# Kernel optimization log

Hardware: AMD Instinct MI355X
Metric: run time of the kernel (lower is better)

## Reference

```python
import jax, jax.numpy as jnp
import numpy as np

B, S, E, H = 4, 1024, 1024, 16
HD = E // H  # head_dim = 64
MAX_SEQ = 1024  # rel positions span [-(MAX_SEQ-1), MAX_SEQ-1]


def setup_inputs() -> dict:
    key = jax.random.key(0)
    ks = jax.random.split(key, 12)
    std_e = 1.0 / np.sqrt(E)
    std_h = 1.0 / np.sqrt(HD)
    inp = {
        "x": jax.random.normal(ks[0], (B, S, E), dtype=jnp.float32),
        # torch nn.Linear weights are [out, in]; y = x @ W.T + b
        "Wq": jax.random.uniform(ks[1], (E, E), jnp.float32, -std_e, std_e),
        "bq": jax.random.uniform(ks[2], (E,), jnp.float32, -std_e, std_e),
        "Wk": jax.random.uniform(ks[3], (E, E), jnp.float32, -std_e, std_e),
        "bk": jax.random.uniform(ks[4], (E,), jnp.float32, -std_e, std_e),
        "Wv": jax.random.uniform(ks[5], (E, E), jnp.float32, -std_e, std_e),
        "bv": jax.random.uniform(ks[6], (E,), jnp.float32, -std_e, std_e),
        "Wo": jax.random.uniform(ks[7], (E, E), jnp.float32, -std_e, std_e),
        "bo": jax.random.uniform(ks[8], (E,), jnp.float32, -std_e, std_e),
        # pos_key_proj: Linear(head_dim, head_dim, bias=False)
        "Wp": jax.random.uniform(ks[9], (HD, HD), jnp.float32, -std_h, std_h),
        # learned relative position table [2*max_seq_len-1, head_dim]
        "rel_table": jax.random.normal(ks[10], (2 * MAX_SEQ - 1, HD), dtype=jnp.float32),
    }
    return inp


def _rel_shift(pos_scores):
    # pos_scores: [B, H, S, 2S-1] -> [B, H, S, S]
    # result[..., i, j] = pos_scores[..., i, (S-1) - i + j]
    s = pos_scores.shape[-2]
    idx = (s - 1) - jnp.arange(s)[:, None] + jnp.arange(s)[None, :]  # [S, S]
    return jnp.take_along_axis(pos_scores, idx[None, None, :, :], axis=-1)


def reference(x, Wq, bq, Wk, bk, Wv, bv, Wo, bo, Wp, rel_table):
    scale = 1.0 / np.sqrt(HD)
    Q = (x @ Wq.T + bq).reshape(B, S, H, HD).transpose(0, 2, 1, 3)  # [B,H,S,HD]
    K = (x @ Wk.T + bk).reshape(B, S, H, HD).transpose(0, 2, 1, 3)
    V = (x @ Wv.T + bv).reshape(B, S, H, HD).transpose(0, 2, 1, 3)

    # rel_pos_encoding(S): slice centered at MAX_SEQ-1 covering 2S-1 positions
    center = MAX_SEQ - 1
    rel_emb = rel_table[center - (S - 1): center + S]  # [2S-1, HD]
    rel_key = rel_emb @ Wp.T                            # [2S-1, HD]

    content = jnp.einsum("bhqd,bhkd->bhqk", Q, K) * scale       # [B,H,S,S]
    pos = jnp.einsum("bhqd,pd->bhqp", Q, rel_key) * scale       # [B,H,S,2S-1]
    scores = content + _rel_shift(pos)                          # [B,H,S,S]

    probs = jax.nn.softmax(scores, axis=-1)
    ctx = jnp.einsum("bhqk,bhkd->bhqd", probs, V)               # [B,H,S,HD]
    ctx = ctx.transpose(0, 2, 1, 3).reshape(B, S, E)
    return ctx @ Wo.T + bo
```

## Files before the change

### kernel.cpp

```cpp
#include <hip/hip_runtime.h>
#include <hip/hip_bf16.h>

#define B_   4
#define S_   1024
#define E_   1024
#define H_   16
#define HD_  64

typedef float  f32x4  __attribute__((ext_vector_type(4)));
typedef short  bf16x8 __attribute__((ext_vector_type(8)));
typedef short  bf16x4 __attribute__((ext_vector_type(4)));

__device__ __forceinline__ float bf2f(short u) {
  union { unsigned int i; float f; } v;
  v.i = ((unsigned int)(unsigned short)u) << 16;
  return v.f;
}
__device__ __forceinline__ short f2bf(float f) {
  unsigned int x = __float_as_uint(f);
  x = x + 0x7fffu + ((x >> 16) & 1u);
  return (short)(x >> 16);
}
__device__ __forceinline__ bf16x8 ld_cvt8(const float* __restrict__ p) {
  const f32x4 a = *(const f32x4*)p;
  const f32x4 b = *(const f32x4*)(p + 4);
  bf16x8 r;
  r[0] = f2bf(a[0]); r[1] = f2bf(a[1]); r[2] = f2bf(a[2]); r[3] = f2bf(a[3]);
  r[4] = f2bf(b[0]); r[5] = f2bf(b[1]); r[6] = f2bf(b[2]); r[7] = f2bf(b[3]);
  return r;
}

__device__ __forceinline__ void gload_lds16(const short* g, short* l) {
  __builtin_amdgcn_global_load_lds(
      (const __attribute__((address_space(1))) void*)g,
      (__attribute__((address_space(3))) void*)l, 16, 0, 0);
}

__global__ __launch_bounds__(256) void cvt_f32_bf16(
    const float* __restrict__ src, short* __restrict__ dst, int n)
{
  const int i = (blockIdx.x * 256 + threadIdx.x) * 4;
  if (i < n) {
    const f32x4 v = *(const f32x4*)(src + i);
    bf16x4 o;
    o[0] = f2bf(v[0]); o[1] = f2bf(v[1]); o[2] = f2bf(v[2]); o[3] = f2bf(v[3]);
    *(bf16x4*)(dst + i) = o;
  }
}

__global__ __launch_bounds__(256) void cvt7_f32_bf16(
    const float* __restrict__ w0, const float* __restrict__ w1,
    const float* __restrict__ w2, const float* __restrict__ x,
    short* __restrict__ WB, short* __restrict__ xbf)
{
  const int NW = E_ * E_;
  const int y = blockIdx.y;
  const float* src;
  short* dst;
  if (y < 3) { src = (y == 0) ? w0 : (y == 1) ? w1 : w2; dst = WB + (size_t)y * NW; }
  else       { src = x + (size_t)(y - 3) * NW;           dst = xbf + (size_t)(y - 3) * NW; }
  const int i = (blockIdx.x * 256 + threadIdx.x) * 4;
  const f32x4 v = *(const f32x4*)(src + i);
  bf16x4 o;
  o[0] = f2bf(v[0]); o[1] = f2bf(v[1]); o[2] = f2bf(v[2]); o[3] = f2bf(v[3]);
  *(bf16x4*)(dst + i) = o;
}

__global__ __launch_bounds__(256, 3) void gemm_qkv(
    const short* __restrict__ A, const short* __restrict__ W012,
    const float* __restrict__ b0, const float* __restrict__ b1, const float* __restrict__ b2,
    short* __restrict__ Qo, short* __restrict__ Ko, short* __restrict__ Vt)
{
  __shared__ short As[128 * 32];
  __shared__ short Bs[3 * 64 * 32];

  const int tid  = threadIdx.x;
  const int lane = tid & 63;
  const int wave = tid >> 6;
  const int quad = lane >> 4;
  const int l15  = lane & 15;
  const int wmb  = (wave >> 1) * 64;
  const int wnb  = (wave & 1) * 32;

  const int lid = blockIdx.x;
  const int m0  = ((lid & 7) * 4 + ((lid >> 3) & 3)) * 128;
  const int n0  = (lid >> 5) * 64;

  const int trow = tid >> 2;
  const int tc   = tid & 3;

  f32x4 acc[3][4][2] = {};

  for (int k0 = 0; k0 < E_; k0 += 32) {
#pragma unroll
    for (int n = 0; n < 2; ++n) {
      const int row  = trow + n * 64;
      const int srcc = tc ^ ((row >> 1) & 3);
      gload_lds16(A + (size_t)(m0 + row) * E_ + k0 + srcc * 8, &As[n * 2048 + tid * 8]);
    }
    {
      const int srcc = tc ^ ((trow >> 1) & 3);
#pragma unroll
      for (int z = 0; z < 3; ++z)
        gload_lds16(W012 + (size_t)z * E_ * E_ + (size_t)(n0 + trow) * E_ + k0 + srcc * 8,
                    &Bs[z * 2048 + tid * 8]);
    }
    __syncthreads();

    bf16x8 af[4];
#pragma unroll
    for (int i = 0; i < 4; ++i) {
      const int row = wmb + i * 16 + l15;
      const int pc  = quad ^ ((row >> 1) & 3);
      af[i] = *(bf16x8*)&As[row * 32 + pc * 8];
    }
#pragma unroll
    for (int z = 0; z < 3; ++z) {
      bf16x8 bfr[2];
#pragma unroll
      for (int j = 0; j < 2; ++j) {
        const int row = wnb + j * 16 + l15;
        const int pc  = quad ^ ((row >> 1) & 3);
        bfr[j] = *(bf16x8*)&Bs[z * 2048 + row * 32 + pc * 8];
      }
#pragma unroll
      for (int i = 0; i < 4; ++i)
#pragma unroll
        for (int j = 0; j < 2; ++j)
          acc[z][i][j] = __builtin_amdgcn_mfma_f32_16x16x32_bf16(af[i], bfr[j], acc[z][i][j], 0, 0, 0);
    }
    __syncthreads();
  }

#pragma unroll
  for (int z = 0; z < 2; ++z) {
    short* C = z ? Ko : Qo;
    const float* bb = z ? b1 : b0;
#pragma unroll
    for (int j = 0; j < 2; ++j) {
      const int n = n0 + wnb + j * 16 + l15;
      const float bv = bb[n];
#pragma unroll
      for (int i = 0; i < 4; ++i) {
        const int m = m0 + wmb + i * 16 + quad * 4;
#pragma unroll
        for (int r = 0; r < 4; ++r)
          C[(size_t)(m + r) * E_ + n] = f2bf(acc[z][i][j][r] + bv);
      }
    }
  }
  {
    const int mtb = m0 + wmb;
    const int bq  = mtb >> 10;
    const int kt  = (mtb >> 6) & 15;
#pragma unroll
    for (int j = 0; j < 2; ++j) {
      const int n = n0 + wnb + j * 16 + l15;
      const float bv = b2[n];
      const int h = (n >> 6) & 15;
      const int d = n & 63;
      bf16x8 lo, hi;
#pragma unroll
      for (int e = 0; e < 8; ++e) {
        lo[e] = f2bf(acc[2][e & 3][j][e >> 2] + bv);
        hi[e] = f2bf(acc[2][e & 3][j][(e >> 2) + 2] + bv);
      }
      const size_t off = ((size_t)((bq * 16 + h) * 64 + d)) * 1024 + kt * 64 + quad * 16;
      *(bf16x8*)(Vt + off)     = lo;
      *(bf16x8*)(Vt + off + 8) = hi;
    }
  }
}

template<int TM, int OUTF32, int XSWZ>
__global__ __launch_bounds__(256) void gemm_bt(
    const short* __restrict__ A,
    const short* __restrict__ W0, const short* __restrict__ W1, const short* __restrict__ W2,
    const float* __restrict__ b0, const float* __restrict__ b1, const float* __restrict__ b2,
    void* __restrict__ C0v, void* __restrict__ C1v, void* __restrict__ C2v, int vz)
{
  constexpr int NJ = (TM == 128) ? 4 : 2;
  __shared__ short As[TM * 32];
  __shared__ short Bs[128 * 32];

  const int tid  = threadIdx.x;
  const int lane = tid & 63;
  const int wave = tid >> 6;
  const int quad = lane >> 4;
  const int l15  = lane & 15;
  const int wmb  = (TM == 128) ? (wave >> 1) * 64 : 0;
  const int wnb  = (TM == 128) ? (wave & 1) * 64 : wave * 32;
  int m0, n0;
  if (XSWZ) {
    const int lid = blockIdx.x;
    m0 = ((lid & 7) * 8 + ((lid >> 3) & 7)) * TM;
    n0 = (lid >> 6) * 128;
  } else {
    m0 = blockIdx.y * TM;
    n0 = blockIdx.x * 128;
  }
  const int z = XSWZ ? 0 : blockIdx.z;

  const short* W  = (z == 0) ? W0 : (z == 1) ? W1 : W2;
  const float* bb = (z == 0) ? b0 : (z == 1) ? b1 : b2;
  void*        Cv = (z == 0) ? C0v : (z == 1) ? C1v : C2v;

  const int trow = tid >> 2;
  const int tc   = tid & 3;

  f32x4 acc[4][NJ] = {};

  for (int k0 = 0; k0 < E_; k0 += 32) {
#pragma unroll
    for (int n = 0; n < TM / 64; ++n) {
      const int row  = trow + n * 64;
      const int srcc = tc ^ ((row >> 1) & 3);
      gload_lds16(A + (size_t)(m0 + row) * E_ + k0 + srcc * 8, &As[n * 2048 + tid * 8]);
    }
#pragma unroll
    for (int n = 0; n < 2; ++n) {
      const int row  = trow + n * 64;
      const int srcc = tc ^ ((row >> 1) & 3);
      gload_lds16(W + (size_t)(n0 + row) * E_ + k0 + srcc * 8, &Bs[n * 2048 + tid * 8]);
    }
    __syncthreads();

    bf16x8 af[4], bfr[NJ];
#pragma unroll
    for (int i = 0; i < 4; ++i) {
      const int row = wmb + i * 16 + l15;
      const int pc  = quad ^ ((row >> 1) & 3);
      af[i] = *(bf16x8*)&As[row * 32 + pc * 8];
    }
#pragma unroll
    for (int j = 0; j < NJ; ++j) {
      const int row = wnb + j * 16 + l15;
      const int pc  = quad ^ ((row >> 1) & 3);
      bfr[j] = *(bf16x8*)&Bs[row * 32 + pc * 8];
    }
#pragma unroll
    for (int i = 0; i < 4; ++i)
#pragma unroll
      for (int j = 0; j < NJ; ++j)
        acc[i][j] = __builtin_amdgcn_mfma_f32_16x16x32_bf16(af[i], bfr[j], acc[i][j], 0, 0, 0);
    __syncthreads();
  }

  if (TM == 128 && z == vz) {
    const int mtb = m0 + wmb;
    const int bq  = mtb >> 10;
    const int kt  = (mtb >> 6) & 15;
    short* Cs = (short*)Cv;
#pragma unroll
    for (int j = 0; j < NJ; ++j) {
      const int n = n0 + wnb + j * 16 + l15;
      const float bv = bb[n];
      const int h = (n >> 6) & 15;
      const int d = n & 63;
      bf16x8 lo, hi;
#pragma unroll
      for (int e = 0; e < 8; ++e) {
        lo[e] = f2bf(acc[e & 3][j][e >> 2] + bv);
        hi[e] = f2bf(acc[e & 3][j][(e >> 2) + 2] + bv);
      }
      const size_t off = ((size_t)((bq * 16 + h) * 64 + d)) * 1024 + kt * 64 + quad * 16;
      *(bf16x8*)(Cs + off)     = lo;
      *(bf16x8*)(Cs + off + 8) = hi;
    }
  } else {
#pragma unroll
    for (int j = 0; j < NJ; ++j) {
      const int n = n0 + wnb + j * 16 + l15;
      const float bv = bb[n];
#pragma unroll
      for (int i = 0; i < 4; ++i) {
        const int m = m0 + wmb + i * 16 + quad * 4;
#pragma unroll
        for (int r = 0; r < 4; ++r) {
          const float v = acc[i][j][r] + bv;
          if (OUTF32) ((float*)Cv)[(size_t)(m + r) * E_ + n] = v;
          else        ((short*)Cv)[(size_t)(m + r) * E_ + n] = f2bf(v);
        }
      }
    }
  }
}

__global__ __launch_bounds__(256) void relkey_mfma(
    const float* __restrict__ rel, const float* __restrict__ Wp, short* __restrict__ RKw)
{
  const int tid  = threadIdx.x;
  const int lane = tid & 63;
  const int wv   = tid >> 6;
  const int quad = lane >> 4;
  const int l15  = lane & 15;
  const int p0   = blockIdx.x * 64 + wv * 16;

  bf16x8 af[2];
  {
    int prow = p0 + l15; if (prow > 2046) prow = 2046;
    const float* ap = rel + (size_t)prow * 64 + quad * 8;
    af[0] = ld_cvt8(ap);
    af[1] = ld_cvt8(ap + 32);
  }
  f32x4 acc[4] = {};
#pragma unroll
  for (int nt = 0; nt < 4; ++nt) {
    const float* bp = Wp + (size_t)(nt * 16 + l15) * 64 + quad * 8;
    acc[nt] = __builtin_amdgcn_mfma_f32_16x16x32_bf16(af[0], ld_cvt8(bp),      acc[nt], 0, 0, 0);
    acc[nt] = __builtin_amdgcn_mfma_f32_16x16x32_bf16(af[1], ld_cvt8(bp + 32), acc[nt], 0, 0, 0);
  }
#pragma unroll
  for (int r = 0; r < 4; ++r) {
    const int p = p0 + quad * 4 + r;
    if (p < 2047)
#pragma unroll
      for (int nt = 0; nt < 4; ++nt)
        RKw[(size_t)p * 64 + nt * 16 + l15] = f2bf(acc[nt][r]);
  }
}

__global__ __launch_bounds__(512, 4) void attn_kernel(
    const short* __restrict__ Qw, const short* __restrict__ Kw,
    const short* __restrict__ Vtg, const short* __restrict__ RKw,
    short* __restrict__ Cw)
{
  __shared__ short Ks[64][72];
  __shared__ short Vt[64][72];
  __shared__ short RKs[256][72];
  __shared__ short Ps[8][16][72];

  const int tid  = threadIdx.x;
  const int lane = tid & 63;
  const int wv   = tid >> 6;
  const int quad = lane >> 4;
  const int l15  = lane & 15;

  const int lid  = blockIdx.x;
  const int pair = (lid & 7) * 8 + (lid >> 6);
  const int qt   = (lid >> 3) & 7;
  const int b    = pair >> 4;
  const int h    = pair & 15;
  const int bh   = pair;
  const int q0   = qt * 128;
  const int qw0  = q0 + wv * 16;
  const int jb   = 112 - 16 * wv;
  const int pbase0 = S_ - 128 - q0;

  bf16x8 qf[2];
  {
    const size_t base = (size_t)(b * S_ + qw0 + l15) * E_ + h * HD_ + quad * 8;
    qf[0] = *(const bf16x8*)(Qw + base);
    qf[1] = *(const bf16x8*)(Qw + base + 32);
  }

  f32x4 oacc[4] = {};
  float lsum[4] = {0.f, 0.f, 0.f, 0.f};

  const float fs = 0.125f * 1.44269504088896340736f;

  const int sr  = tid >> 3;
  const int sc8 = (tid & 7) * 8;

  {
    *(bf16x8*)&Ks[sr][sc8] =
        *(const bf16x8*)(Kw + (size_t)(b * S_ + sr) * E_ + h * HD_ + sc8);
    *(bf16x8*)&Vt[sr][sc8] =
        *(const bf16x8*)(Vtg + (size_t)(bh * 64 + sr) * 1024 + sc8);
#pragma unroll
    for (int jj = 0; jj < 3; ++jj) {
      const int c = tid + jj * 512;
      const int row = c >> 3, ch = (c & 7) * 8;
      int p = pbase0 + row; p = (p > 2046) ? 2046 : p;
      *(bf16x8*)&RKs[row][ch] = *(const bf16x8*)(RKw + (size_t)p * 64 + ch);
    }
    __syncthreads();
  }

#pragma unroll 1
  for (int kt = 0; kt < 16; ++kt) {
    bf16x8 kreg, vreg, rkreg;
    const bool havekv = (kt < 15);
    const bool haverk = (kt < 15);
    if (havekv) {
      kreg = *(const bf16x8*)(Kw + (size_t)(b * S_ + (kt + 1) * 64 + sr) * E_ + h * HD_ + sc8);
      vreg = *(const bf16x8*)(Vtg + (size_t)(bh * 64 + sr) * 1024 + (kt + 1) * 64 + sc8);
    }
    if (haverk) {
      int p = pbase0 + 64 * (kt + 3) + sr; if (p > 2046) p = 2046;
      rkreg = *(const bf16x8*)(RKw + (size_t)p * 64 + sc8);
    }

    f32x4 sc[4] = {};
#pragma unroll
    for (int s = 0; s < 2; ++s) {
#pragma unroll
      for (int kk = 0; kk < 4; ++kk) {
        bf16x8 bf = *(bf16x8*)&Ks[kk*16 + l15][s*32 + quad*8];
        sc[kk] = __builtin_amdgcn_mfma_f32_16x16x32_bf16(qf[s], bf, sc[kk], 0, 0, 0);
      }
    }

    f32x4 ta[5] = {};
#pragma unroll
    for (int jt = 0; jt < 5; ++jt) {
      const int off  = jb + jt * 16;
      const int slot = (kt + (off >> 6)) & 3;
      const int prow = slot * 64 + (off & 63);
#pragma unroll
      for (int s = 0; s < 2; ++s) {
        bf16x8 bf = *(bf16x8*)&RKs[prow + l15][s*32 + quad*8];
        ta[jt] = __builtin_amdgcn_mfma_f32_16x16x32_bf16(qf[s], bf, ta[jt], 0, 0, 0);
      }
    }

    float p[4][4];
#pragma unroll
    for (int r = 0; r < 4; ++r) {
      const int i16 = quad*4 + r;
      const int d   = 15 + l15 - i16;
      const int srcLane = (quad << 4) | (d & 15);
      float sj[5];
#pragma unroll
      for (int jt = 0; jt < 5; ++jt) sj[jt] = __shfl(ta[jt][r], srcLane, 64);
      const bool hi = (d >= 16);
#pragma unroll
      for (int kk = 0; kk < 4; ++kk) {
        const float t = hi ? sj[kk+1] : sj[kk];
        const float sv = fminf((sc[kk][r] + t) * fs, 108.f);
        const float pv = exp2f(sv - 12.f);
        p[kk][r] = pv;
        lsum[r] += pv;
      }
    }

#pragma unroll
    for (int r = 0; r < 4; ++r) {
      bf16x4 pw;
      pw[0] = f2bf(p[0][r]); pw[1] = f2bf(p[1][r]);
      pw[2] = f2bf(p[2][r]); pw[3] = f2bf(p[3][r]);
      *(bf16x4*)&Ps[wv][quad*4 + r][l15*4] = pw;
    }

#pragma unroll
    for (int ks = 0; ks < 2; ++ks) {
      bf16x8 pa = *(bf16x8*)&Ps[wv][l15][ks*32 + quad*8];
#pragma unroll
      for (int dt = 0; dt < 4; ++dt) {
        bf16x8 vb = *(bf16x8*)&Vt[dt*16 + l15][ks*32 + quad*8];
        oacc[dt] = __builtin_amdgcn_mfma_f32_16x16x32_bf16(pa, vb, oacc[dt], 0, 0, 0);
      }
    }

    __syncthreads();
    if (havekv) {
      *(bf16x8*)&Ks[sr][sc8] = kreg;
      *(bf16x8*)&Vt[sr][sc8] = vreg;
    }
    if (haverk) {
      *(bf16x8*)&RKs[((kt + 3) & 3) * 64 + sr][sc8] = rkreg;
    }
    __syncthreads();
  }

#pragma unroll
  for (int off = 1; off <= 8; off <<= 1)
#pragma unroll
    for (int r = 0; r < 4; ++r)
      lsum[r] += __shfl_xor(lsum[r], off, 64);

#pragma unroll
  for (int r = 0; r < 4; ++r) {
    const float inv = 1.0f / lsum[r];
    const size_t row = (size_t)(b * S_ + qw0 + quad*4 + r) * E_ + h * HD_;
#pragma unroll
    for (int dt = 0; dt < 4; ++dt)
      Cw[row + dt*16 + l15] = f2bf(oacc[dt][r] * inv);
  }
}

__global__ void fill_kernel(float* __restrict__ out, int n, float val) {
  for (int i = blockIdx.x * blockDim.x + threadIdx.x; i < n; i += gridDim.x * blockDim.x)
    out[i] = val;
}

extern "C" void kernel_launch(void* const* d_in, const int* in_sizes, int n_in,
                              void* d_out, int out_size, void* d_ws, size_t ws_size,
                              hipStream_t stream)
{
  const size_t WS_NEEDED = 33816448;
  if (ws_size < WS_NEEDED) {
    fill_kernel<<<1024, 256, 0, stream>>>((float*)d_out, out_size, 0.25f);
    return;
  }
  if (n_in != 11 || in_sizes[10] != 2047 * 64) {
    fill_kernel<<<1024, 256, 0, stream>>>((float*)d_out, out_size, 0.75f);
    return;
  }

  const float* x   = (const float*)d_in[0];
  const float* Wq  = (const float*)d_in[1];
  const float* bq  = (const float*)d_in[2];
  const float* Wk  = (const float*)d_in[3];
  const float* bk  = (const float*)d_in[4];
  const float* Wv  = (const float*)d_in[5];
  const float* bv  = (const float*)d_in[6];
  const float* Wo  = (const float*)d_in[7];
  const float* bo  = (const float*)d_in[8];
  const float* Wp  = (const float*)d_in[9];
  const float* rel = (const float*)d_in[10];

  char* ws = (char*)d_ws;
  short* Qws = (short*)(ws);
  short* Kws = (short*)(ws + 8388608);
  short* Vtg = (short*)(ws + 16777216);
  short* WB  = (short*)(ws + 25165824);
  short* ctx = (short*)(ws + 25165824);
  short* WoB = (short*)(ws + 8388608);
  short* RKw = (short*)(ws + 33554432);
  short* xbf = (short*)d_out;

  const int NW = E_ * E_;

  cvt7_f32_bf16<<<dim3(1024, 7), dim3(256), 0, stream>>>(Wq, Wk, Wv, x, WB, xbf);

  gemm_qkv<<<dim3(512), dim3(256), 0, stream>>>(
      xbf, WB, bq, bk, bv, Qws, Kws, Vtg);

  relkey_mfma<<<dim3(32), dim3(256), 0, stream>>>(rel, Wp, RKw);

  attn_kernel<<<dim3(512), dim3(512), 0, stream>>>(Qws, Kws, Vtg, RKw, ctx);

  cvt_f32_bf16<<<dim3(NW / 1024), dim3(256), 0, stream>>>(Wo, WoB, NW);

  gemm_bt<64, 1, 1><<<dim3(512), dim3(256), 0, stream>>>(
      ctx, WoB, WoB, WoB, bo, bo, bo, d_out, d_out, d_out, -1);
}
```

Baseline: 242.2 us.

## Double-buffer GEMM LDS loads and fold preprocessing into one prep kernel

Adds double-buffered LDS staging to the QKV and output-projection GEMMs, so the next K-slice is loaded while the current one goes through MFMA, and drops one barrier per iteration. Merges the Wo conversion and the relative-key projection into the single prep launch, cutting the launch count from six to four. The attention output now overwrites the Q buffer in place, so the restrict qualifiers on those pointers were removed. This doubles LDS per block, which may reduce occupancy, and the in-place write is only safe if each tile's Q is read before its ctx is written.

```diff
diff --git a/kernel.cpp b/kernel.cpp
--- a/kernel.cpp
+++ b/kernel.cpp
@@ -36,29 +36,56 @@
       (__attribute__((address_space(3))) void*)l, 16, 0, 0);
 }
 
-__global__ __launch_bounds__(256) void cvt_f32_bf16(
-    const float* __restrict__ src, short* __restrict__ dst, int n)
-{
-  const int i = (blockIdx.x * 256 + threadIdx.x) * 4;
-  if (i < n) {
-    const f32x4 v = *(const f32x4*)(src + i);
-    bf16x4 o;
-    o[0] = f2bf(v[0]); o[1] = f2bf(v[1]); o[2] = f2bf(v[2]); o[3] = f2bf(v[3]);
-    *(bf16x4*)(dst + i) = o;
-  }
-}
-
-__global__ __launch_bounds__(256) void cvt7_f32_bf16(
+__global__ __launch_bounds__(256) void prep_kernel(
     const float* __restrict__ w0, const float* __restrict__ w1,
     const float* __restrict__ w2, const float* __restrict__ x,
-    short* __restrict__ WB, short* __restrict__ xbf)
+    const float* __restrict__ wo, const float* __restrict__ rel,
+    const float* __restrict__ Wp,
+    short* __restrict__ WB, short* __restrict__ xbf,
+    short* __restrict__ WoB, short* __restrict__ RKw)
 {
   const int NW = E_ * E_;
-  const int y = blockIdx.y;
+  const int y  = blockIdx.y;
+
+  if (y == 8) {
+    if (blockIdx.x >= 32) return;
+    const int tid  = threadIdx.x;
+    const int lane = tid & 63;
+    const int wv   = tid >> 6;
+    const int quad = lane >> 4;
+    const int l15  = lane & 15;
+    const int p0   = blockIdx.x * 64 + wv * 16;
+
+    bf16x8 af[2];
+    {
+      int prow = p0 + l15; if (prow > 2046) prow = 2046;
+      const float* ap = rel + (size_t)prow * 64 + quad * 8;
+      af[0] = ld_cvt8(ap);
+      af[1] = ld_cvt8(ap + 32);
+    }
+    f32x4 acc[4] = {};
+#pragma unroll
+    for (int nt = 0; nt < 4; ++nt) {
+      const float* bp = Wp + (size_t)(nt * 16 + l15) * 64 + quad * 8;
+      acc[nt] = __builtin_amdgcn_mfma_f32_16x16x32_bf16(af[0], ld_cvt8(bp),      acc[nt], 0, 0, 0);
+      acc[nt] = __builtin_amdgcn_mfma_f32_16x16x32_bf16(af[1], ld_cvt8(bp + 32), acc[nt], 0, 0, 0);
+    }
+#pragma unroll
+    for (int r = 0; r < 4; ++r) {
+      const int p = p0 + quad * 4 + r;
+      if (p < 2047)
+#pragma unroll
+        for (int nt = 0; nt < 4; ++nt)
+          RKw[(size_t)p * 64 + nt * 16 + l15] = f2bf(acc[nt][r]);
+    }
+    return;
+  }
+
   const float* src;
   short* dst;
-  if (y < 3) { src = (y == 0) ? w0 : (y == 1) ? w1 : w2; dst = WB + (size_t)y * NW; }
-  else       { src = x + (size_t)(y - 3) * NW;           dst = xbf + (size_t)(y - 3) * NW; }
+  if (y < 3)      { src = (y == 0) ? w0 : (y == 1) ? w1 : w2; dst = WB + (size_t)y * NW; }
+  else if (y < 7) { src = x + (size_t)(y - 3) * NW;           dst = xbf + (size_t)(y - 3) * NW; }
+  else            { src = wo;                                  dst = WoB; }
   const int i = (blockIdx.x * 256 + threadIdx.x) * 4;
   const f32x4 v = *(const f32x4*)(src + i);
   bf16x4 o;
@@ -71,8 +98,8 @@
     const float* __restrict__ b0, const float* __restrict__ b1, const float* __restrict__ b2,
     short* __restrict__ Qo, short* __restrict__ Ko, short* __restrict__ Vt)
 {
-  __shared__ short As[128 * 32];
-  __shared__ short Bs[3 * 64 * 32];
+  __shared__ short As[2][128 * 32];
+  __shared__ short Bs[2][3 * 64 * 32];
 
   const int tid  = threadIdx.x;
   const int lane = tid & 63;
@@ -89,30 +116,37 @@
   const int trow = tid >> 2;
   const int tc   = tid & 3;
 
-  f32x4 acc[3][4][2] = {};
-
-  for (int k0 = 0; k0 < E_; k0 += 32) {
+  auto stage = [&](int k0, int bsel) {
 #pragma unroll
     for (int n = 0; n < 2; ++n) {
       const int row  = trow + n * 64;
       const int srcc = tc ^ ((row >> 1) & 3);
-      gload_lds16(A + (size_t)(m0 + row) * E_ + k0 + srcc * 8, &As[n * 2048 + tid * 8]);
-    }
-    {
-      const int srcc = tc ^ ((trow >> 1) & 3);
-#pragma unroll
-      for (int z = 0; z < 3; ++z)
-        gload_lds16(W012 + (size_t)z * E_ * E_ + (size_t)(n0 + trow) * E_ + k0 + srcc * 8,
-                    &Bs[z * 2048 + tid * 8]);
-    }
-    __syncthreads();
+      gload_lds16(A + (size_t)(m0 + row) * E_ + k0 + srcc * 8,
+                  &As[bsel][n * 2048 + tid * 8]);
+    }
+    const int srcc = tc ^ ((trow >> 1) & 3);
+#pragma unroll
+    for (int z = 0; z < 3; ++z)
+      gload_lds16(W012 + (size_t)z * E_ * E_ + (size_t)(n0 + trow) * E_ + k0 + srcc * 8,
+                  &Bs[bsel][z * 2048 + tid * 8]);
+  };
+
+  f32x4 acc[3][4][2] = {};
+
+  stage(0, 0);
+  __syncthreads();
+
+#pragma unroll 2
+  for (int t = 0; t < 32; ++t) {
+    const int cur = t & 1;
+    if (t < 31) stage((t + 1) * 32, cur ^ 1);
 
     bf16x8 af[4];
 #pragma unroll
     for (int i = 0; i < 4; ++i) {
       const int row = wmb + i * 16 + l15;
       const int pc  = quad ^ ((row >> 1) & 3);
-      af[i] = *(bf16x8*)&As[row * 32 + pc * 8];
+      af[i] = *(bf16x8*)&As[cur][row * 32 + pc * 8];
     }
 #pragma unroll
     for (int z = 0; z < 3; ++z) {
@@ -121,7 +155,7 @@
       for (int j = 0; j < 2; ++j) {
         const int row = wnb + j * 16 + l15;
         const int pc  = quad ^ ((row >> 1) & 3);
-        bfr[j] = *(bf16x8*)&Bs[z * 2048 + row * 32 + pc * 8];
+        bfr[j] = *(bf16x8*)&Bs[cur][z * 2048 + row * 32 + pc * 8];
       }
 #pragma unroll
       for (int i = 0; i < 4; ++i)
@@ -172,158 +206,89 @@
   }
 }
 
-template<int TM, int OUTF32, int XSWZ>
-__global__ __launch_bounds__(256) void gemm_bt(
-    const short* __restrict__ A,
-    const short* __restrict__ W0, const short* __restrict__ W1, const short* __restrict__ W2,
-    const float* __restrict__ b0, const float* __restrict__ b1, const float* __restrict__ b2,
-    void* __restrict__ C0v, void* __restrict__ C1v, void* __restrict__ C2v, int vz)
+__global__ __launch_bounds__(256) void gemm_out(
+    const short* __restrict__ A, const short* __restrict__ W,
+    const float* __restrict__ bb, float* __restrict__ C)
 {
-  constexpr int NJ = (TM == 128) ? 4 : 2;
-  __shared__ short As[TM * 32];
-  __shared__ short Bs[128 * 32];
+  __shared__ short As[2][64 * 32];
+  __shared__ short Bs[2][128 * 32];
 
   const int tid  = threadIdx.x;
   const int lane = tid & 63;
   const int wave = tid >> 6;
   const int quad = lane >> 4;
   const int l15  = lane & 15;
-  const int wmb  = (TM == 128) ? (wave >> 1) * 64 : 0;
-  const int wnb  = (TM == 128) ? (wave & 1) * 64 : wave * 32;
-  int m0, n0;
-  if (XSWZ) {
-    const int lid = blockIdx.x;
-    m0 = ((lid & 7) * 8 + ((lid >> 3) & 7)) * TM;
-    n0 = (lid >> 6) * 128;
-  } else {
-    m0 = blockIdx.y * TM;
-    n0 = blockIdx.x * 128;
-  }
-  const int z = XSWZ ? 0 : blockIdx.z;
-
-  const short* W  = (z == 0) ? W0 : (z == 1) ? W1 : W2;
-  const float* bb = (z == 0) ? b0 : (z == 1) ? b1 : b2;
-  void*        Cv = (z == 0) ? C0v : (z == 1) ? C1v : C2v;
+  const int wnb  = wave * 32;
+
+  const int lid = blockIdx.x;
+  const int m0  = ((lid & 7) * 8 + ((lid >> 3) & 7)) * 64;
+  const int n0  = (lid >> 6) * 128;
 
   const int trow = tid >> 2;
   const int tc   = tid & 3;
 
-  f32x4 acc[4][NJ] = {};
-
-  for (int k0 = 0; k0 < E_; k0 += 32) {
-#pragma unroll
-    for (int n = 0; n < TM / 64; ++n) {
-      const int row  = trow + n * 64;
-      const int srcc = tc ^ ((row >> 1) & 3);
-      gload_lds16(A + (size_t)(m0 + row) * E_ + k0 + srcc * 8, &As[n * 2048 + tid * 8]);
+  auto stage = [&](int k0, int bsel) {
+    {
+      const int srcc = tc ^ ((trow >> 1) & 3);
+      gload_lds16(A + (size_t)(m0 + trow) * E_ + k0 + srcc * 8, &As[bsel][tid * 8]);
     }
 #pragma unroll
     for (int n = 0; n < 2; ++n) {
       const int row  = trow + n * 64;
       const int srcc = tc ^ ((row >> 1) & 3);
-      gload_lds16(W + (size_t)(n0 + row) * E_ + k0 + srcc * 8, &Bs[n * 2048 + tid * 8]);
-    }
-    __syncthreads();
-
-    bf16x8 af[4], bfr[NJ];
+      gload_lds16(W + (size_t)(n0 + row) * E_ + k0 + srcc * 8, &Bs[bsel][n * 2048 + tid * 8]);
+    }
+  };
+
+  f32x4 acc[4][2] = {};
+
+  stage(0, 0);
+  __syncthreads();
+
+#pragma unroll 2
+  for (int t = 0; t < 32; ++t) {
+    const int cur = t & 1;
+    if (t < 31) stage((t + 1) * 32, cur ^ 1);
+
+    bf16x8 af[4], bfr[2];
 #pragma unroll
     for (int i = 0; i < 4; ++i) {
-      const int row = wmb + i * 16 + l15;
+      const int row = i * 16 + l15;
       const int pc  = quad ^ ((row >> 1) & 3);
-      af[i] = *(bf16x8*)&As[row * 32 + pc * 8];
-    }
-#pragma unroll
-    for (int j = 0; j < NJ; ++j) {
+      af[i] = *(bf16x8*)&As[cur][row * 32 + pc * 8];
+    }
+#pragma unroll
+    for (int j = 0; j < 2; ++j) {
       const int row = wnb + j * 16 + l15;
       const int pc  = quad ^ ((row >> 1) & 3);
-      bfr[j] = *(bf16x8*)&Bs[row * 32 + pc * 8];
+      bfr[j] = *(bf16x8*)&Bs[cur][row * 32 + pc * 8];
     }
 #pragma unroll
     for (int i = 0; i < 4; ++i)
 #pragma unroll
-      for (int j = 0; j < NJ; ++j)
+      for (int j = 0; j < 2; ++j)
         acc[i][j] = __builtin_amdgcn_mfma_f32_16x16x32_bf16(af[i], bfr[j], acc[i][j], 0, 0, 0);
     __syncthreads();
   }
 
-  if (TM == 128 && z == vz) {
-    const int mtb = m0 + wmb;
-    const int bq  = mtb >> 10;
-    const int kt  = (mtb >> 6) & 15;
-    short* Cs = (short*)Cv;
-#pragma unroll
-    for (int j = 0; j < NJ; ++j) {
-      const int n = n0 + wnb + j * 16 + l15;
-      const float bv = bb[n];
-      const int h = (n >> 6) & 15;
-      const int d = n & 63;
-      bf16x8 lo, hi;
-#pragma unroll
-      for (int e = 0; e < 8; ++e) {
-        lo[e] = f2bf(acc[e & 3][j][e >> 2] + bv);
-        hi[e] = f2bf(acc[e & 3][j][(e >> 2) + 2] + bv);
-      }
-      const size_t off = ((size_t)((bq * 16 + h) * 64 + d)) * 1024 + kt * 64 + quad * 16;
-      *(bf16x8*)(Cs + off)     = lo;
-      *(bf16x8*)(Cs + off + 8) = hi;
-    }
-  } else {
-#pragma unroll
-    for (int j = 0; j < NJ; ++j) {
-      const int n = n0 + wnb + j * 16 + l15;
-      const float bv = bb[n];
-#pragma unroll
-      for (int i = 0; i < 4; ++i) {
-        const int m = m0 + wmb + i * 16 + quad * 4;
-#pragma unroll
-        for (int r = 0; r < 4; ++r) {
-          const float v = acc[i][j][r] + bv;
-          if (OUTF32) ((float*)Cv)[(size_t)(m + r) * E_ + n] = v;
-          else        ((short*)Cv)[(size_t)(m + r) * E_ + n] = f2bf(v);
-        }
-      }
-    }
-  }
-}
-
-__global__ __launch_bounds__(256) void relkey_mfma(
-    const float* __restrict__ rel, const float* __restrict__ Wp, short* __restrict__ RKw)
-{
-  const int tid  = threadIdx.x;
-  const int lane = tid & 63;
-  const int wv   = tid >> 6;
-  const int quad = lane >> 4;
-  const int l15  = lane & 15;
-  const int p0   = blockIdx.x * 64 + wv * 16;
-
-  bf16x8 af[2];
-  {
-    int prow = p0 + l15; if (prow > 2046) prow = 2046;
-    const float* ap = rel + (size_t)prow * 64 + quad * 8;
-    af[0] = ld_cvt8(ap);
-    af[1] = ld_cvt8(ap + 32);
-  }
-  f32x4 acc[4] = {};
-#pragma unroll
-  for (int nt = 0; nt < 4; ++nt) {
-    const float* bp = Wp + (size_t)(nt * 16 + l15) * 64 + quad * 8;
-    acc[nt] = __builtin_amdgcn_mfma_f32_16x16x32_bf16(af[0], ld_cvt8(bp),      acc[nt], 0, 0, 0);
-    acc[nt] = __builtin_amdgcn_mfma_f32_16x16x32_bf16(af[1], ld_cvt8(bp + 32), acc[nt], 0, 0, 0);
-  }
-#pragma unroll
-  for (int r = 0; r < 4; ++r) {
-    const int p = p0 + quad * 4 + r;
-    if (p < 2047)
-#pragma unroll
-      for (int nt = 0; nt < 4; ++nt)
-        RKw[(size_t)p * 64 + nt * 16 + l15] = f2bf(acc[nt][r]);
+#pragma unroll
+  for (int j = 0; j < 2; ++j) {
+    const int n = n0 + wnb + j * 16 + l15;
+    const float bv = bb[n];
+#pragma unroll
+    for (int i = 0; i < 4; ++i) {
+      const int m = m0 + i * 16 + quad * 4;
+#pragma unroll
+      for (int r = 0; r < 4; ++r)
+        C[(size_t)(m + r) * E_ + n] = acc[i][j][r] + bv;
+    }
   }
 }
 
 __global__ __launch_bounds__(512, 4) void attn_kernel(
-    const short* __restrict__ Qw, const short* __restrict__ Kw,
+    const short* Qw, const short* __restrict__ Kw,
     const short* __restrict__ Vtg, const short* __restrict__ RKw,
-    short* __restrict__ Cw)
+    short* Cw)
 {
   __shared__ short Ks[64][72];
   __shared__ short Vt[64][72];
@@ -515,24 +480,17 @@
   short* Kws = (short*)(ws + 8388608);
   short* Vtg = (short*)(ws + 16777216);
   short* WB  = (short*)(ws + 25165824);
-  short* ctx = (short*)(ws + 25165824);
-  short* WoB = (short*)(ws + 8388608);
+  short* WoB = (short*)(ws + 31457280);
   short* RKw = (short*)(ws + 33554432);
   short* xbf = (short*)d_out;
 
-  const int NW = E_ * E_;
-
-  cvt7_f32_bf16<<<dim3(1024, 7), dim3(256), 0, stream>>>(Wq, Wk, Wv, x, WB, xbf);
+  prep_kernel<<<dim3(1024, 9), dim3(256), 0, stream>>>(
+      Wq, Wk, Wv, x, Wo, rel, Wp, WB, xbf, WoB, RKw);
 
   gemm_qkv<<<dim3(512), dim3(256), 0, stream>>>(
       xbf, WB, bq, bk, bv, Qws, Kws, Vtg);
 
-  relkey_mfma<<<dim3(32), dim3(256), 0, stream>>>(rel, Wp, RKw);
-
-  attn_kernel<<<dim3(512), dim3(512), 0, stream>>>(Qws, Kws, Vtg, RKw, ctx);
-
-  cvt_f32_bf16<<<dim3(NW / 1024), dim3(256), 0, stream>>>(Wo, WoB, NW);
-
-  gemm_bt<64, 1, 1><<<dim3(512), dim3(256), 0, stream>>>(
-      ctx, WoB, WoB, WoB, bo, bo, bo, d_out, d_out, d_out, -1);
-}
+  attn_kernel<<<dim3(512), dim3(512), 0, stream>>>(Qws, Kws, Vtg, RKw, Qws);
+
+  gemm_out<<<dim3(512), dim3(256), 0, stream>>>(Qws, WoB, bo, (float*)d_out);
+}
```

Result: no change. 238.5 us (-1.5%).
